# Optimization experiments

Measured on AMD Instinct MI355X. Metric: run time of the kernel, lower is better.

The kernel has to match this reference:

```python
import jax, jax.numpy as jnp
import numpy as np

# Faithful math of the torch module (dropout in eval mode => identity):
#   alpha = sigmoid(smoothing_weight)                       # [h,1] -> [1,1,h,1]
#   out[t] = alpha^(t+1) * v0 + sum_{s<=t} (1-alpha) alpha^(t-s) * values[s]
#   aux path kernel: weight/clamp(1-alpha,1e-6)*alpha => factor*alpha^(t-s+1)
#     with factor = (1-alpha)/max(1-alpha,1e-6) (== 1 unless alpha ~ 1)
# The torch code realizes this causal linear recurrence via FFT cross-correlation;
# here we use an associative (parallel) scan, which computes the same sums.

B, T, H, D = 8, 4096, 8, 64

def setup_inputs() -> dict:
    key = jax.random.key(0)
    k1, k2, k3, k4 = jax.random.split(key, 4)
    values = jax.random.normal(k1, (B, T, H, D), dtype=jnp.float32)
    aux_values = jax.random.normal(k2, (B, T, H, D), dtype=jnp.float32)
    v0 = jax.random.normal(k3, (1, 1, H, D), dtype=jnp.float32)
    smoothing_weight = jax.random.normal(k4, (H, 1), dtype=jnp.float32)
    return {"values": values, "aux_values": aux_values, "v0": v0,
            "smoothing_weight": smoothing_weight}

def reference(values, aux_values, v0, smoothing_weight):
    b, t, h, d = values.shape
    alpha = jax.nn.sigmoid(smoothing_weight).reshape(1, 1, h, 1)  # [1,1,h,1]
    one_m = 1.0 - alpha
    factor = one_m / jnp.maximum(one_m, 1e-6)  # == 1 unless alpha ~ 1 (clamp in torch)
    # Linear recurrence y[t] = alpha*y[t-1] + u[t], y[-1] = v0, where
    # u[t] = (1-alpha)*values[t] + factor*alpha*aux_values[t] (fused main + aux path).
    a = jnp.broadcast_to(alpha, (1, t, h, 1))               # decay coeffs
    u = one_m * values + (factor * alpha) * aux_values      # [b,t,h,d]
    def combine(c1, c2):
        a1, b1 = c1
        a2, b2 = c2
        return (a1 * a2, a2 * b1 + b2)
    A, Bsum = jax.lax.associative_scan(combine, (a, u), axis=1)
    # A[t] = alpha^(t+1); Bsum[t] = sum_{s<=t} alpha^(t-s) * u[s]
    return A * v0 + Bsum
```

## Files before the change

### kernel.cpp

```cpp
#include <hip/hip_runtime.h>
#include <math.h>

#define BB 8
#define TT 4096
#define HH 8
#define DD 64
#define NC 256
#define LL (TT / NC)

__device__ __forceinline__ float sigmoidf_(float x) {
    return 1.0f / (1.0f + expf(-x));
}

__global__ __launch_bounds__(128)
void k_partial(const float4* __restrict__ vals, const float4* __restrict__ aux,
               const float* __restrict__ w, float4* __restrict__ out,
               float4* __restrict__ Z) {
    const int blk = blockIdx.x;
    const int b = blk / NC, c = blk % NC;
    const int tid = threadIdx.x;
    const int h = tid >> 4;

    const float alpha = sigmoidf_(w[h]);
    const float onem  = 1.0f - alpha;
    const float fa    = (onem / fmaxf(onem, 1e-6f)) * alpha;

    int base = (b * TT + c * LL) * 128 + tid;

    float4 y = make_float4(0.f, 0.f, 0.f, 0.f);
#pragma unroll
    for (int i = 0; i < LL; ++i) {
        float4 v = vals[base + i * 128];
        float4 a = aux[base + i * 128];
        y.x = alpha * y.x + (onem * v.x + fa * a.x);
        y.y = alpha * y.y + (onem * v.y + fa * a.y);
        y.z = alpha * y.z + (onem * v.z + fa * a.z);
        y.w = alpha * y.w + (onem * v.w + fa * a.w);
        out[base + i * 128] = y;
    }
    Z[(b * NC + c) * 128 + tid] = y;
}

__global__ __launch_bounds__(256)
void k_scan(const float4* __restrict__ Z, const float* __restrict__ v0,
            const float* __restrict__ w, float4* __restrict__ P) {
    __shared__ float lds[NC][33];

    const int blk = blockIdx.x;
    const int b  = blk >> 4;
    const int h  = (blk >> 1) & 7;
    const int dh = blk & 1;
    const int r4base = h * 16 + dh * 8;
    const int tid = threadIdx.x;

    const float alpha = sigmoidf_(w[h]);
    const float aL = powf(alpha, (float)LL);

#pragma unroll
    for (int it = 0; it < 8; ++it) {
        int idx = it * 256 + tid;
        int c = idx >> 3, k = idx & 7;
        float4 z = Z[(b * NC + c) * 128 + r4base + k];
        lds[c][k * 4 + 0] = z.x;
        lds[c][k * 4 + 1] = z.y;
        lds[c][k * 4 + 2] = z.z;
        lds[c][k * 4 + 3] = z.w;
    }
    __syncthreads();

    const int c = tid;
    float s[32];
#pragma unroll
    for (int k = 0; k < 32; ++k) s[k] = lds[c][k];

    float m = aL;
    for (int off = 1; off < NC; off <<= 1) {
        float tmp[32];
        const bool act = (c >= off);
        if (act) {
#pragma unroll
            for (int k = 0; k < 32; ++k) tmp[k] = lds[c - off][k];
        }
        __syncthreads();
        if (act) {
#pragma unroll
            for (int k = 0; k < 32; ++k) { s[k] += m * tmp[k]; lds[c][k] = s[k]; }
        }
        m *= m;
        __syncthreads();
    }

    const float pc = powf(alpha, (float)(LL * c));
    const float4* v04 = (const float4*)v0;
#pragma unroll
    for (int k = 0; k < 8; ++k) {
        float4 vv = v04[r4base + k];
        float4 pr;
        if (c == 0) {
            pr = vv;
        } else {
            pr.x = pc * vv.x + lds[c - 1][k * 4 + 0];
            pr.y = pc * vv.y + lds[c - 1][k * 4 + 1];
            pr.z = pc * vv.z + lds[c - 1][k * 4 + 2];
            pr.w = pc * vv.w + lds[c - 1][k * 4 + 3];
        }
        P[(b * NC + c) * 128 + r4base + k] = pr;
    }
}

__global__ __launch_bounds__(128)
void k_final(const float* __restrict__ w, const float4* __restrict__ P,
             float4* __restrict__ out) {
    const int blk = blockIdx.x;
    const int b = blk / NC, c = blk % NC;
    const int tid = threadIdx.x;
    const int h = tid >> 4;

    const float alpha = sigmoidf_(w[h]);
    const float4 p = P[(b * NC + c) * 128 + tid];
    int base = (b * TT + c * LL) * 128 + tid;

    float coef = alpha;
#pragma unroll
    for (int i = 0; i < LL; ++i) {
        float4 o = out[base + i * 128];
        o.x += coef * p.x;
        o.y += coef * p.y;
        o.z += coef * p.z;
        o.w += coef * p.w;
        out[base + i * 128] = o;
        coef *= alpha;
    }
}

extern "C" void kernel_launch(void* const* d_in, const int* in_sizes, int n_in,
                              void* d_out, int out_size, void* d_ws, size_t ws_size,
                              hipStream_t stream) {
    const float4* vals = (const float4*)d_in[0];
    const float4* aux  = (const float4*)d_in[1];
    const float*  v0   = (const float*)d_in[2];
    const float*  w    = (const float*)d_in[3];
    float4* out = (float4*)d_out;

    float4* Z = (float4*)d_ws;
    float4* P = Z + (size_t)BB * NC * 128;

    k_partial<<<BB * NC, 128, 0, stream>>>(vals, aux, w, out, Z);
    k_scan<<<BB * HH * 2, 256, 0, stream>>>(Z, v0, w, P);
    k_final<<<BB * NC, 128, 0, stream>>>(w, P, out);
}
```

Baseline: 196.2 us.

## Switch to reduce-then-scan with input recompute and non-temporal output stores

Result: no change. 198.1 us (+1.0%).

```diff
diff --git a/kernel.cpp b/kernel.cpp
--- a/kernel.cpp
+++ b/kernel.cpp
@@ -5,19 +5,20 @@
 #define TT 4096
 #define HH 8
 #define DD 64
-#define NC 256
-#define LL (TT / NC)
+
+typedef float f32x4_native __attribute__((ext_vector_type(4)));
 
 __device__ __forceinline__ float sigmoidf_(float x) {
     return 1.0f / (1.0f + expf(-x));
 }
 
+template<int NCv>
 __global__ __launch_bounds__(128)
-void k_partial(const float4* __restrict__ vals, const float4* __restrict__ aux,
-               const float* __restrict__ w, float4* __restrict__ out,
-               float4* __restrict__ Z) {
+void k_agg(const float4* __restrict__ vals, const float4* __restrict__ aux,
+           const float* __restrict__ w, float4* __restrict__ Z) {
+    constexpr int L = TT / NCv;
     const int blk = blockIdx.x;
-    const int b = blk / NC, c = blk % NC;
+    const int b = blk / NCv, c = blk % NCv;
     const int tid = threadIdx.x;
     const int h = tid >> 4;
 
@@ -25,42 +26,50 @@
     const float onem  = 1.0f - alpha;
     const float fa    = (onem / fmaxf(onem, 1e-6f)) * alpha;
 
-    int base = (b * TT + c * LL) * 128 + tid;
+    int base = (b * TT + c * L) * 128 + tid;
 
     float4 y = make_float4(0.f, 0.f, 0.f, 0.f);
 #pragma unroll
-    for (int i = 0; i < LL; ++i) {
-        float4 v = vals[base + i * 128];
-        float4 a = aux[base + i * 128];
-        y.x = alpha * y.x + (onem * v.x + fa * a.x);
-        y.y = alpha * y.y + (onem * v.y + fa * a.y);
-        y.z = alpha * y.z + (onem * v.z + fa * a.z);
-        y.w = alpha * y.w + (onem * v.w + fa * a.w);
-        out[base + i * 128] = y;
+    for (int hh = 0; hh < L / 8; ++hh) {
+        float4 v[8], a[8];
+#pragma unroll
+        for (int i = 0; i < 8; ++i) {
+            v[i] = vals[base + (hh * 8 + i) * 128];
+            a[i] = aux [base + (hh * 8 + i) * 128];
+        }
+#pragma unroll
+        for (int i = 0; i < 8; ++i) {
+            y.x = alpha * y.x + (onem * v[i].x + fa * a[i].x);
+            y.y = alpha * y.y + (onem * v[i].y + fa * a[i].y);
+            y.z = alpha * y.z + (onem * v[i].z + fa * a[i].z);
+            y.w = alpha * y.w + (onem * v[i].w + fa * a[i].w);
+        }
     }
-    Z[(b * NC + c) * 128 + tid] = y;
+    Z[(b * NCv + c) * 128 + tid] = y;
 }
 
-__global__ __launch_bounds__(256)
+template<int NCv>
+__global__ __launch_bounds__(512)
 void k_scan(const float4* __restrict__ Z, const float* __restrict__ v0,
             const float* __restrict__ w, float4* __restrict__ P) {
-    __shared__ float lds[NC][33];
+    constexpr int L = TT / NCv;
+    __shared__ float lds[NCv][9];
 
     const int blk = blockIdx.x;
-    const int b  = blk >> 4;
-    const int h  = (blk >> 1) & 7;
-    const int dh = blk & 1;
-    const int r4base = h * 16 + dh * 8;
+    const int b  = blk >> 6;
+    const int h  = (blk >> 3) & 7;
+    const int d8 = blk & 7;
+    const int r4 = h * 16 + d8 * 2;
     const int tid = threadIdx.x;
 
     const float alpha = sigmoidf_(w[h]);
-    const float aL = powf(alpha, (float)LL);
+    const float aL = powf(alpha, (float)L);
 
 #pragma unroll
-    for (int it = 0; it < 8; ++it) {
-        int idx = it * 256 + tid;
-        int c = idx >> 3, k = idx & 7;
-        float4 z = Z[(b * NC + c) * 128 + r4base + k];
+    for (int it = 0; it < 2; ++it) {
+        int idx = it * NCv + tid;
+        int c = idx >> 1, k = idx & 1;
+        float4 z = Z[(b * NCv + c) * 128 + r4 + k];
         lds[c][k * 4 + 0] = z.x;
         lds[c][k * 4 + 1] = z.y;
         lds[c][k * 4 + 2] = z.z;
@@ -69,32 +78,32 @@
     __syncthreads();
 
     const int c = tid;
-    float s[32];
+    float s[8];
 #pragma unroll
-    for (int k = 0; k < 32; ++k) s[k] = lds[c][k];
+    for (int k = 0; k < 8; ++k) s[k] = lds[c][k];
 
     float m = aL;
-    for (int off = 1; off < NC; off <<= 1) {
-        float tmp[32];
+    for (int off = 1; off < NCv; off <<= 1) {
+        float tmp[8];
         const bool act = (c >= off);
         if (act) {
 #pragma unroll
-            for (int k = 0; k < 32; ++k) tmp[k] = lds[c - off][k];
+            for (int k = 0; k < 8; ++k) tmp[k] = lds[c - off][k];
         }
         __syncthreads();
         if (act) {
 #pragma unroll
-            for (int k = 0; k < 32; ++k) { s[k] += m * tmp[k]; lds[c][k] = s[k]; }
+            for (int k = 0; k < 8; ++k) { s[k] += m * tmp[k]; lds[c][k] = s[k]; }
         }
         m *= m;
         __syncthreads();
     }
 
-    const float pc = powf(alpha, (float)(LL * c));
+    const float pc = powf(alpha, (float)(L * c));
     const float4* v04 = (const float4*)v0;
 #pragma unroll
-    for (int k = 0; k < 8; ++k) {
-        float4 vv = v04[r4base + k];
+    for (int k = 0; k < 2; ++k) {
+        float4 vv = v04[r4 + k];
         float4 pr;
         if (c == 0) {
             pr = vv;
@@ -104,32 +113,53 @@
             pr.z = pc * vv.z + lds[c - 1][k * 4 + 2];
             pr.w = pc * vv.w + lds[c - 1][k * 4 + 3];
         }
-        P[(b * NC + c) * 128 + r4base + k] = pr;
+        P[(b * NCv + c) * 128 + r4 + k] = pr;
     }
 }
 
+template<int NCv>
 __global__ __launch_bounds__(128)
-void k_final(const float* __restrict__ w, const float4* __restrict__ P,
-             float4* __restrict__ out) {
+void k_out(const float4* __restrict__ vals, const float4* __restrict__ aux,
+           const float* __restrict__ w, const float4* __restrict__ P,
+           float4* __restrict__ out) {
+    constexpr int L = TT / NCv;
     const int blk = blockIdx.x;
-    const int b = blk / NC, c = blk % NC;
+    const int b = blk / NCv, c = blk % NCv;
     const int tid = threadIdx.x;
     const int h = tid >> 4;
 
     const float alpha = sigmoidf_(w[h]);
-    const float4 p = P[(b * NC + c) * 128 + tid];
-    int base = (b * TT + c * LL) * 128 + tid;
+    const float onem  = 1.0f - alpha;
+    const float fa    = (onem / fmaxf(onem, 1e-6f)) * alpha;
 
+    const float4 p = P[(b * NCv + c) * 128 + tid];
+    int base = (b * TT + c * L) * 128 + tid;
+
+    float4 y = make_float4(0.f, 0.f, 0.f, 0.f);
     float coef = alpha;
 #pragma unroll
-    for (int i = 0; i < LL; ++i) {
-        float4 o = out[base + i * 128];
-        o.x += coef * p.x;
-        o.y += coef * p.y;
-        o.z += coef * p.z;
-        o.w += coef * p.w;
-        out[base + i * 128] = o;
-        coef *= alpha;
+    for (int hh = 0; hh < L / 8; ++hh) {
+        float4 v[8], a[8];
+#pragma unroll
+        for (int i = 0; i < 8; ++i) {
+            v[i] = vals[base + (hh * 8 + i) * 128];
+            a[i] = aux [base + (hh * 8 + i) * 128];
+        }
+#pragma unroll
+        for (int i = 0; i < 8; ++i) {
+            y.x = alpha * y.x + (onem * v[i].x + fa * a[i].x);
+            y.y = alpha * y.y + (onem * v[i].y + fa * a[i].y);
+            y.z = alpha * y.z + (onem * v[i].z + fa * a[i].z);
+            y.w = alpha * y.w + (onem * v[i].w + fa * a[i].w);
+            float4 o;
+            o.x = y.x + coef * p.x;
+            o.y = y.y + coef * p.y;
+            o.z = y.z + coef * p.z;
+            o.w = y.w + coef * p.w;
+            __builtin_nontemporal_store(*(const f32x4_native*)&o,
+                                        (f32x4_native*)&out[base + (hh * 8 + i) * 128]);
+            coef *= alpha;
+        }
     }
 }
 
@@ -140,12 +170,24 @@
     const float4* aux  = (const float4*)d_in[1];
     const float*  v0   = (const float*)d_in[2];
     const float*  w    = (const float*)d_in[3];
+
     float4* out = (float4*)d_out;
 
-    float4* Z = (float4*)d_ws;
-    float4* P = Z + (size_t)BB * NC * 128;
+    const size_t need512 = 2ull * BB * 512 * 128 * sizeof(float4);
 
-    k_partial<<<BB * NC, 128, 0, stream>>>(vals, aux, w, out, Z);
-    k_scan<<<BB * HH * 2, 256, 0, stream>>>(Z, v0, w, P);
-    k_final<<<BB * NC, 128, 0, stream>>>(w, P, out);
+    if (ws_size >= need512) {
+        constexpr int NCv = 512;
+        float4* Z = (float4*)d_ws;
+        float4* P = Z + (size_t)BB * NCv * 128;
+        k_agg <NCv><<<BB * NCv,   128, 0, stream>>>(vals, aux, w, Z);
+        k_scan<NCv><<<BB * HH * 8, NCv, 0, stream>>>(Z, v0, w, P);
+        k_out <NCv><<<BB * NCv,   128, 0, stream>>>(vals, aux, w, P, out);
+    } else {
+        constexpr int NCv = 256;
+        float4* Z = (float4*)d_ws;
+        float4* P = Z + (size_t)BB * NCv * 128;
+        k_agg <NCv><<<BB * NCv,   128, 0, stream>>>(vals, aux, w, Z);
+        k_scan<NCv><<<BB * HH * 8, NCv, 0, stream>>>(Z, v0, w, P);
+        k_out <NCv><<<BB * NCv,   128, 0, stream>>>(vals, aux, w, P, out);
+    }
 }
```
